# Kernel tuning notes

Hardware: AMD Instinct MI355X
Metric: run time of the kernel (lower is better)

Reference implementation:

```python
import jax, jax.numpy as jnp
import numpy as np

N_NODES = 50000
N_EDGES = 800000
BATCH = 128
D_IN = 768
D_H = 256
EPS_BN = 1e-5
EPS_COS = 1e-8


def setup_inputs() -> dict:
    key = jax.random.key(0)
    ks = jax.random.split(key, 16)
    s = 0.05
    return {
        "claim_embeddings": jax.random.normal(ks[0], (BATCH, D_IN), jnp.float32),
        "x": jax.random.normal(ks[1], (N_NODES, D_IN), jnp.float32),
        "edge_index": jax.random.randint(ks[2], (2, N_EDGES), 0, N_NODES, jnp.int32),
        "batch": jnp.sort(jax.random.randint(ks[3], (N_NODES,), 0, BATCH, jnp.int32)),
        "W1": jax.random.normal(ks[4], (D_IN, D_H), jnp.float32) * s,
        "a_src1": jax.random.normal(ks[5], (D_H,), jnp.float32) * s,
        "a_dst1": jax.random.normal(ks[6], (D_H,), jnp.float32) * s,
        "b1": jnp.zeros((D_H,), jnp.float32),
        "W2": jax.random.normal(ks[7], (D_H, D_H), jnp.float32) * s,
        "a_src2": jax.random.normal(ks[8], (D_H,), jnp.float32) * s,
        "a_dst2": jax.random.normal(ks[9], (D_H,), jnp.float32) * s,
        "b2": jnp.zeros((D_H,), jnp.float32),
        "bn_gamma": jnp.ones((D_H,), jnp.float32),
        "bn_beta": jnp.zeros((D_H,), jnp.float32),
        "Wc": jax.random.normal(ks[10], (D_H + D_IN, 1), jnp.float32) * s,
        "bc": jnp.zeros((1,), jnp.float32),
    }


def _gat_layer(h_in, src, dst, W, a_s, a_d, b, n_nodes):
    """PyG GATConv (heads=1, concat=True, self-loops already in src/dst)."""
    h = h_in @ W                                   # [N, D_H]
    alpha_s = h @ a_s                               # [N]
    alpha_d = h @ a_d                               # [N]
    e = jax.nn.leaky_relu(alpha_s[src] + alpha_d[dst], 0.2)  # [E+N]
    # numerically-stable softmax segmented by destination node
    e = e - jax.ops.segment_max(e, dst, num_segments=n_nodes)[dst]
    w = jnp.exp(e)
    w = w / jax.ops.segment_sum(w, dst, num_segments=n_nodes)[dst]
    out = jax.ops.segment_sum(h[src] * w[:, None], dst, num_segments=n_nodes)
    return out + b


def reference(claim_embeddings, x, edge_index, batch,
              W1, a_src1, a_dst1, b1, W2, a_src2, a_dst2, b2,
              bn_gamma, bn_beta, Wc, bc):
    n = x.shape[0]
    n_graphs = claim_embeddings.shape[0]
    # cosine-similarity relevance gating (torch eps semantics)
    ce = claim_embeddings[batch]                    # [N, D_IN]
    denom = jnp.maximum(jnp.linalg.norm(ce, axis=-1) * jnp.linalg.norm(x, axis=-1), EPS_COS)
    rel = jnp.sum(ce * x, axis=-1) / denom          # [N]
    h = x * rel[:, None]
    # add self-loops once (GATConv default add_self_loops=True)
    loops = jnp.arange(n, dtype=edge_index.dtype)
    src = jnp.concatenate([edge_index[0], loops])
    dst = jnp.concatenate([edge_index[1], loops])
    # layer 1 + batchnorm (batch stats) + relu
    h = _gat_layer(h, src, dst, W1, a_src1, a_dst1, b1, n)
    mean = jnp.mean(h, axis=0)
    var = jnp.mean(jnp.square(h - mean), axis=0)
    h = bn_gamma * (h - mean) * jax.lax.rsqrt(var + EPS_BN) + bn_beta
    h = jax.nn.relu(h)
    # layer 2 + relu
    h = _gat_layer(h, src, dst, W2, a_src2, a_dst2, b2, n)
    h = jax.nn.relu(h)
    # global mean pool per graph
    sums = jax.ops.segment_sum(h, batch, num_segments=n_graphs)
    counts = jax.ops.segment_sum(jnp.ones((n,), h.dtype), batch, num_segments=n_graphs)
    pooled = sums / jnp.maximum(counts, 1.0)[:, None]   # [B, D_H]
    combined = jnp.concatenate([pooled, claim_embeddings], axis=1)  # [B, D_H+D_IN]
    out = combined @ Wc + bc                        # [B, 1]
    return out.squeeze(-1)
```

## Files before the change

kernel.cpp:

```cpp
#include <hip/hip_runtime.h>
#include <hip/hip_bf16.h>

#define DIN 768
#define DH  256

typedef unsigned short ushort_t;
typedef unsigned char uchar_t;
typedef __attribute__((ext_vector_type(8))) short short8v;
typedef __attribute__((ext_vector_type(4))) float f32x4;
typedef __attribute__((ext_vector_type(2))) float f32x2;

__host__ __device__ inline int orig_col(int s) {
  int u = (s >> 2) & 31;
  return (s & ~127) | (((u >> 4) & 1) << 6) | ((s & 3) << 4) | (u & 15);
}

__device__ inline float wave_sum(float v) {
#pragma unroll
  for (int o = 32; o; o >>= 1) v += __shfl_xor(v, o);
  return v;
}
__device__ inline void wave_sum2(float& a, float& b) {
#pragma unroll
  for (int o = 32; o; o >>= 1) {
    a += __shfl_xor(a, o);
    b += __shfl_xor(b, o);
  }
}
__device__ inline float leaky(float v) { return v > 0.f ? v : 0.2f * v; }

__device__ inline ushort_t f2bf(float f) {
  union { float f; unsigned u; } v; v.f = f;
  unsigned r = v.u + 0x7FFFu + ((v.u >> 16) & 1u);
  return (ushort_t)(r >> 16);
}
__device__ inline float bf2f(ushort_t u) {
  union { unsigned u; float f; } t; t.u = ((unsigned)u) << 16; return t.f;
}

__device__ inline void unpack16f8(uint4 v, float* f) {
  f32x2 p;
  p = __builtin_amdgcn_cvt_pk_f32_fp8(v.x, false); f[0] = p[0]; f[1] = p[1];
  p = __builtin_amdgcn_cvt_pk_f32_fp8(v.x, true);  f[2] = p[0]; f[3] = p[1];
  p = __builtin_amdgcn_cvt_pk_f32_fp8(v.y, false); f[4] = p[0]; f[5] = p[1];
  p = __builtin_amdgcn_cvt_pk_f32_fp8(v.y, true);  f[6] = p[0]; f[7] = p[1];
  p = __builtin_amdgcn_cvt_pk_f32_fp8(v.z, false); f[8] = p[0]; f[9] = p[1];
  p = __builtin_amdgcn_cvt_pk_f32_fp8(v.z, true);  f[10] = p[0]; f[11] = p[1];
  p = __builtin_amdgcn_cvt_pk_f32_fp8(v.w, false); f[12] = p[0]; f[13] = p[1];
  p = __builtin_amdgcn_cvt_pk_f32_fp8(v.w, true);  f[14] = p[0]; f[15] = p[1];
}
__device__ inline uint4 pack8(const float* f) {
  uint4 o;
  o.x = (unsigned)f2bf(f[0]) | ((unsigned)f2bf(f[1]) << 16);
  o.y = (unsigned)f2bf(f[2]) | ((unsigned)f2bf(f[3]) << 16);
  o.z = (unsigned)f2bf(f[4]) | ((unsigned)f2bf(f[5]) << 16);
  o.w = (unsigned)f2bf(f[6]) | ((unsigned)f2bf(f[7]) << 16);
  return o;
}

__global__ __launch_bounds__(256) void relxb_hist_kernel(
    const float* __restrict__ ce, const float* __restrict__ x,
    const int* __restrict__ batch, const float* __restrict__ cenorm,
    ushort_t* __restrict__ xb, float* __restrict__ rel, int n,
    const int* __restrict__ edst, int E, int* __restrict__ cnt) {
  int node = blockIdx.x * 4 + (threadIdx.x >> 6);
  int lane = threadIdx.x & 63;
  if (node < n) {
    int g = batch[node];
    const float4* xr = (const float4*)(x + (size_t)node * DIN);
    const float4* cr = (const float4*)(ce + (size_t)g * DIN);
    float dxy = 0.f, dxx = 0.f;
#pragma unroll
    for (int i = 0; i < 3; i++) {
      float4 a = xr[lane + 64 * i];
      float4 b = cr[lane + 64 * i];
      ushort4 o = make_ushort4(f2bf(a.x), f2bf(a.y), f2bf(a.z), f2bf(a.w));
      *(ushort4*)&xb[(size_t)node * DIN + (lane + 64 * i) * 4] = o;
      dxy += a.x*b.x + a.y*b.y + a.z*b.z + a.w*b.w;
      dxx += a.x*a.x + a.y*a.y + a.z*a.z + a.w*a.w;
    }
    wave_sum2(dxy, dxx);
    if (lane == 0) {
      float denom = fmaxf(sqrtf(dxx) * cenorm[g], 1e-8f);
      rel[node] = dxy / denom;
    }
  }
  for (int e = blockIdx.x * blockDim.x + threadIdx.x; e < E;
       e += gridDim.x * blockDim.x)
    atomicAdd(&cnt[edst[e]], 1);
}

__global__ __launch_bounds__(256) void prep_kernel(
    const float* __restrict__ W1, const float* __restrict__ W2,
    const float* __restrict__ b1, const float* __restrict__ b2,
    const float* __restrict__ gamma, const float* __restrict__ beta,
    const float* __restrict__ Wc, const float* __restrict__ ce,
    ushort_t* __restrict__ Wt1, ushort_t* __restrict__ Wt2,
    float* __restrict__ pb1, float* __restrict__ pb2,
    float* __restrict__ pgamma, float* __restrict__ pbeta,
    float* __restrict__ pWc, float* __restrict__ cenorm, int B) {
  __shared__ float tile[64][65];
  int b = blockIdx.x;
  int t = threadIdx.x;
  int r4 = t >> 6;
  int c64 = t & 63;
  if (b < 48) {
    int k0 = (b % 12) * 64, c0 = (b / 12) * 64;
#pragma unroll
    for (int rr = 0; rr < 16; rr++) {
      int r = rr * 4 + r4;
      tile[r][c64] = W1[(size_t)(k0 + r) * 256 + c0 + c64];
    }
    __syncthreads();
#pragma unroll
    for (int rr = 0; rr < 16; rr++) {
      int cc = rr * 4 + r4;
      Wt1[(size_t)(c0 + cc) * DIN + k0 + c64] = f2bf(tile[c64][cc]);
    }
  } else if (b < 64) {
    int bb = b - 48;
    int k0 = (bb & 3) * 64, c0 = (bb >> 2) * 64;
#pragma unroll
    for (int rr = 0; rr < 16; rr++) {
      int r = rr * 4 + r4;
      tile[r][c64] = W2[(size_t)orig_col(k0 + r) * 256 + c0 + c64];
    }
    __syncthreads();
#pragma unroll
    for (int rr = 0; rr < 16; rr++) {
      int cc = rr * 4 + r4;
      Wt2[(size_t)(c0 + cc) * DH + k0 + c64] = f2bf(tile[c64][cc]);
    }
  } else if (b == 64) {
    int o = orig_col(t);
    pb1[t] = b1[o];
    pb2[t] = b2[o];
    pgamma[t] = gamma[o];
    pbeta[t] = beta[o];
    pWc[t] = Wc[o];
  } else {
    int lane = t & 63;
    for (int g = r4; g < B; g += 4) {
      const float4* cr = (const float4*)(ce + (size_t)g * DIN);
      float s = 0.f;
#pragma unroll
      for (int i = 0; i < 3; i++) {
        float4 v = cr[lane + 64 * i];
        s += v.x*v.x + v.y*v.y + v.z*v.z + v.w*v.w;
      }
      s = wave_sum(s);
      if (lane == 0) cenorm[g] = sqrtf(s);
    }
  }
}

__global__ __launch_bounds__(256) void scan1_kernel(const int* __restrict__ cnt,
                                                    int* __restrict__ row_off,
                                                    int* __restrict__ bsum, int n) {
  __shared__ int s[256];
  int t = threadIdx.x;
  int i = blockIdx.x * 256 + t;
  int v = (i < n) ? cnt[i] : 0;
  s[t] = v;
  __syncthreads();
  for (int off = 1; off < 256; off <<= 1) {
    int tmp = (t >= off) ? s[t - off] : 0;
    __syncthreads();
    s[t] += tmp;
    __syncthreads();
  }
  if (i < n) row_off[i] = s[t] - v;
  if (t == 255) bsum[blockIdx.x] = s[255];
}

__global__ __launch_bounds__(256) void scan2_kernel(const int* __restrict__ bsum,
                                                    int* __restrict__ boff, int nb,
                                                    int* __restrict__ row_off, int n) {
  __shared__ int s[256];
  int t = threadIdx.x;
  int v = (t < nb) ? bsum[t] : 0;
  s[t] = v;
  __syncthreads();
  for (int off = 1; off < 256; off <<= 1) {
    int tmp = (t >= off) ? s[t - off] : 0;
    __syncthreads();
    s[t] += tmp;
    __syncthreads();
  }
  if (t < nb) boff[t] = s[t] - v;
  if (t == nb - 1) row_off[n] = s[t];
}

__global__ __launch_bounds__(256) void scan3_kernel(int* __restrict__ row_off,
                                                    const int* __restrict__ boff, int n) {
  int i = blockIdx.x * 256 + threadIdx.x;
  if (i < n) row_off[i] += boff[blockIdx.x];
}

__global__ void fill_kernel(const int* __restrict__ src, const int* __restrict__ dst, int E,
                            const int* __restrict__ row_off, int* __restrict__ fill,
                            int* __restrict__ col_src) {
  for (int e = blockIdx.x * blockDim.x + threadIdx.x; e < E; e += gridDim.x * blockDim.x) {
    int d = dst[e];
    int slot = row_off[d] + atomicAdd(&fill[d], 1);
    col_src[slot] = src[e];
  }
}

template <int K>
__global__ __launch_bounds__(256) void gemm_mfma(
    const ushort_t* __restrict__ A, const ushort_t* __restrict__ Bt,
    uchar_t* __restrict__ C, const float* __restrict__ scale,
    const float* __restrict__ a_s, const float* __restrict__ a_d,
    float* __restrict__ alpha_s, float* __restrict__ alpha_d, int Mreal) {
  __shared__ ushort_t lds[16384];
  const int tid = threadIdx.x;
  const int lane = tid & 63;
  const int wave = tid >> 6;

  int p = blockIdx.y * 2 + blockIdx.x;
  int total = 2 * gridDim.y;
  int cch = p >> 4;
  int v;
  if ((cch << 4) + 16 <= total) {
    int r = p & 15;
    v = (cch << 4) | ((r & 7) << 1) | (r >> 3);
  } else {
    v = p;
  }
  const int col0 = (v & 1) * 128;
  const int row0 = (v >> 1) * 128;

  const int wr = wave >> 1, wc = wave & 1;
  const int c16 = lane & 15, g4 = lane >> 4;
  const int st_roff = lane >> 3;
  const int st_gsrc = (lane & 7) ^ st_roff;

  f32x4 acc[4][4];
#pragma unroll
  for (int m = 0; m < 4; m++)
#pragma unroll
    for (int nn = 0; nn < 4; nn++)
#pragma unroll
      for (int j = 0; j < 4; j++) acc[m][nn][j] = 0.f;

  for (int k0 = 0; k0 < K; k0 += 64) {
#pragma unroll
    for (int ci = 0; ci < 8; ci++) {
      int inst = wave * 8 + ci;
      int isB = inst >> 4;
      int idx = inst & 15;
      int lrow = idx * 8 + st_roff;
      const ushort_t* gsrc;
      if (isB == 0) {
        int rg = row0 + lrow;
        rg = rg < Mreal ? rg : Mreal - 1;
        gsrc = A + (size_t)rg * K + k0 + st_gsrc * 8;
      } else {
        gsrc = Bt + (size_t)(col0 + lrow) * K + k0 + st_gsrc * 8;
      }
      __builtin_amdgcn_global_load_lds(
          (const __attribute__((address_space(1))) void*)gsrc,
          (__attribute__((address_space(3))) void*)&lds[isB * 8192 + idx * 512],
          16, 0, 0);
    }
    __syncthreads();
#pragma unroll
    for (int ks = 0; ks < 2; ks++) {
      int g = ks * 4 + g4;
      short8v a[4], b[4];
#pragma unroll
      for (int m = 0; m < 4; m++) {
        int ra = wr * 64 + m * 16 + c16;
        a[m] = *(const short8v*)&lds[ra * 64 + (g ^ (ra & 7)) * 8];
      }
#pragma unroll
      for (int nn = 0; nn < 4; nn++) {
        int rb = wc * 64 + nn * 16 + c16;
        b[nn] = *(const short8v*)&lds[8192 + rb * 64 + (g ^ (rb & 7)) * 8];
      }
#pragma unroll
      for (int m = 0; m < 4; m++)
#pragma unroll
        for (int nn = 0; nn < 4; nn++)
          acc[m][nn] = __builtin_amdgcn_mfma_f32_16x16x32_bf16(a[m], b[nn],
                                                               acc[m][nn], 0, 0, 0);
    }
    __syncthreads();
  }

  float asv[4], adv[4];
#pragma unroll
  for (int nn = 0; nn < 4; nn++) {
    int col = col0 + wc * 64 + nn * 16 + c16;
    asv[nn] = a_s[col];
    adv[nn] = a_d[col];
  }

  uint* Cw = (uint*)C;
#pragma unroll
  for (int m = 0; m < 4; m++) {
    int row_base = row0 + wr * 64 + m * 16 + g4 * 4;
#pragma unroll
    for (int j = 0; j < 4; j++) {
      int row = row_base + j;
      int rc = row < Mreal ? row : Mreal - 1;
      float s = scale ? scale[rc] : 1.0f;
      float vs[4];
      float ps = 0.f, pd = 0.f;
#pragma unroll
      for (int nn = 0; nn < 4; nn++) {
        float v2 = acc[m][nn][j] * s;
        vs[nn] = v2;
        ps = fmaf(v2, asv[nn], ps);
        pd = fmaf(v2, adv[nn], pd);
      }
#pragma unroll
      for (int o = 1; o < 16; o <<= 1) {
        ps += __shfl_xor(ps, o);
        pd += __shfl_xor(pd, o);
      }
      if (c16 == 0 && row < Mreal) {
        atomicAdd(&alpha_s[row], ps);
        atomicAdd(&alpha_d[row], pd);
      }
      if (row < Mreal) {
        unsigned w8 = __builtin_amdgcn_cvt_pk_fp8_f32(vs[0], vs[1], 0u, false);
        w8 = __builtin_amdgcn_cvt_pk_fp8_f32(vs[2], vs[3], w8, true);
        Cw[(size_t)row * 64 + (col0 >> 2) + wc * 16 + c16] = w8;
      }
    }
  }
}

__global__ __launch_bounds__(256) void gat_agg(
    const uchar_t* __restrict__ h8, const float* __restrict__ as_,
    const float* __restrict__ ad_, const int* __restrict__ row_off,
    const int* __restrict__ col_src, const float* __restrict__ bias,
    ushort_t* __restrict__ outb, int n, int relu_out) {
  int node = blockIdx.x * 4 + (threadIdx.x >> 6);
  int lane = threadIdx.x & 63;
  if (node >= n) return;
  int lo = row_off[node], hi = row_off[node + 1];
  int deg = hi - lo;
  float adn = ad_[node];
  float w_self = __expf(leaky(as_[node] + adn));

  const int q = lane >> 4;
  const int l16 = lane & 15;
  const uchar_t* rowbase = h8 + (size_t)l16 * 16;

  float acc[16];
  float zacc = (lane == 0) ? w_self : 0.f;
  {
    uint4 v = *(const uint4*)(rowbase + (size_t)node * 256);
    float ws = (q == 0) ? w_self : 0.f;
    float f[16];
    unpack16f8(v, f);
#pragma unroll
    for (int i = 0; i < 16; i++) acc[i] = ws * f[i];
  }

  for (int base = 0; base < deg; base += 64) {
    int cnt = min(64, deg - base);
    int s = 0; float w = 0.f;
    if (lane < cnt) {
      s = col_src[lo + base + lane];
      w = __expf(leaky(as_[s] + adn));
    }
    zacc += w;
    int e = 0;
    for (; e + 8 <= cnt; e += 8) {
      int iA = e + q, iB = e + 4 + q;
      int sA = __shfl(s, iA);
      float wA = __shfl(w, iA);
      int sB = __shfl(s, iB);
      float wB = __shfl(w, iB);
      uint4 a0 = *(const uint4*)(rowbase + (size_t)sA * 256);
      uint4 b0 = *(const uint4*)(rowbase + (size_t)sB * 256);
      float f[16];
      unpack16f8(a0, f);
#pragma unroll
      for (int i = 0; i < 16; i++) acc[i] = fmaf(wA, f[i], acc[i]);
      unpack16f8(b0, f);
#pragma unroll
      for (int i = 0; i < 16; i++) acc[i] = fmaf(wB, f[i], acc[i]);
    }
    for (; e < cnt; e += 4) {
      int myE = e + q;
      int idx = myE < cnt ? myE : cnt - 1;
      int ss = __shfl(s, idx);
      float wv = __shfl(w, idx);
      float wgt = (myE < cnt) ? wv : 0.f;
      uint4 v = *(const uint4*)(rowbase + (size_t)ss * 256);
      float f[16];
      unpack16f8(v, f);
#pragma unroll
      for (int i = 0; i < 16; i++) acc[i] = fmaf(wgt, f[i], acc[i]);
    }
  }

  float z = wave_sum(zacc);
  float inv_z = 1.0f / z;

#pragma unroll
  for (int i = 0; i < 16; i++) {
    acc[i] += __shfl_xor(acc[i], 16);
    acc[i] += __shfl_xor(acc[i], 32);
  }

  if (q == 0) {
    float o[16];
#pragma unroll
    for (int i = 0; i < 16; i += 4) {
      float4 bb = *(const float4*)&bias[l16 * 16 + i];
      o[i]     = fmaf(acc[i],     inv_z, bb.x);
      o[i + 1] = fmaf(acc[i + 1], inv_z, bb.y);
      o[i + 2] = fmaf(acc[i + 2], inv_z, bb.z);
      o[i + 3] = fmaf(acc[i + 3], inv_z, bb.w);
    }
    if (relu_out) {
#pragma unroll
      for (int i = 0; i < 16; i++) o[i] = fmaxf(o[i], 0.f);
    }
    uint4* op = (uint4*)(outb + (size_t)node * 256 + l16 * 16);
    op[0] = pack8(o);
    op[1] = pack8(o + 8);
  }
}

__global__ __launch_bounds__(256) void bn_stats(const ushort_t* __restrict__ h, int n,
                                                float* __restrict__ bsum,
                                                float* __restrict__ bsq) {
  int c = threadIdx.x;
  int rows_per_block = (n + gridDim.x - 1) / gridDim.x;
  int r0 = blockIdx.x * rows_per_block;
  int r1 = min(r0 + rows_per_block, n);
  float sum = 0.f, sq = 0.f;
  for (int r = r0; r < r1; r++) {
    float v = bf2f(h[(size_t)r * 256 + c]);
    sum += v;
    sq = fmaf(v, v, sq);
  }
  atomicAdd(&bsum[c], sum);
  atomicAdd(&bsq[c], sq);
}

__global__ __launch_bounds__(256) void bn_apply(const ushort_t* __restrict__ h,
                                                const float* __restrict__ bsum,
                                                const float* __restrict__ bsq,
                                                const float* __restrict__ gamma,
                                                const float* __restrict__ beta,
                                                ushort_t* __restrict__ h2b, int n) {
  int total4 = n * 64;
  float inv_n = 1.0f / (float)n;
  for (int f = blockIdx.x * blockDim.x + threadIdx.x; f < total4;
       f += gridDim.x * blockDim.x) {
    int c4 = f & 63;
    uint2 hv = ((const uint2*)h)[f];
    float v0, v1, v2, v3;
    {
      union { unsigned u; float fl; } t;
      t.u = hv.x << 16;         v0 = t.fl;
      t.u = hv.x & 0xFFFF0000u; v1 = t.fl;
      t.u = hv.y << 16;         v2 = t.fl;
      t.u = hv.y & 0xFFFF0000u; v3 = t.fl;
    }
    float4 sm = ((const float4*)bsum)[c4];
    float4 sl = ((const float4*)bsq)[c4];
    float4 g = ((const float4*)gamma)[c4];
    float4 bb = ((const float4*)beta)[c4];
    float m, var;
    m = sm.x * inv_n; var = sl.x * inv_n - m * m;
    v0 = fmaxf(g.x * (v0 - m) * rsqrtf(var + 1e-5f) + bb.x, 0.f);
    m = sm.y * inv_n; var = sl.y * inv_n - m * m;
    v1 = fmaxf(g.y * (v1 - m) * rsqrtf(var + 1e-5f) + bb.y, 0.f);
    m = sm.z * inv_n; var = sl.z * inv_n - m * m;
    v2 = fmaxf(g.z * (v2 - m) * rsqrtf(var + 1e-5f) + bb.z, 0.f);
    m = sm.w * inv_n; var = sl.w * inv_n - m * m;
    v3 = fmaxf(g.w * (v3 - m) * rsqrtf(var + 1e-5f) + bb.w, 0.f);
    uint2 o;
    o.x = (unsigned)f2bf(v0) | ((unsigned)f2bf(v1) << 16);
    o.y = (unsigned)f2bf(v2) | ((unsigned)f2bf(v3) << 16);
    ((uint2*)h2b)[f] = o;
  }
}

__device__ inline int lower_bound_dev(const int* a, int n, int v) {
  int lo = 0, hi = n;
  while (lo < hi) {
    int mid = (lo + hi) >> 1;
    if (a[mid] < v) lo = mid + 1; else hi = mid;
  }
  return lo;
}

#define POOL_CHUNKS 16
__global__ __launch_bounds__(256) void pool_partial(const ushort_t* __restrict__ h,
                                                    const int* __restrict__ batch, int n,
                                                    float* __restrict__ psum) {
  int g = blockIdx.x / POOL_CHUNKS;
  int c = blockIdx.x % POOL_CHUNKS;
  int lo = lower_bound_dev(batch, n, g);
  int hi = lower_bound_dev(batch, n, g + 1);
  int len = hi - lo;
  int r0 = lo + (int)(((long long)len * c) / POOL_CHUNKS);
  int r1 = lo + (int)(((long long)len * (c + 1)) / POOL_CHUNKS);
  if (r1 <= r0) return;
  float sum = 0.f;
  for (int r = r0; r < r1; r++) sum += bf2f(h[(size_t)r * 256 + threadIdx.x]);
  atomicAdd(&psum[(size_t)g * 256 + threadIdx.x], sum);
}

__global__ __launch_bounds__(256) void final_kernel(const float* __restrict__ psum,
                                                    const int* __restrict__ batch, int n,
                                                    const float* __restrict__ ce,
                                                    const float* __restrict__ pWc,
                                                    const float* __restrict__ Wc,
                                                    const float* __restrict__ bc,
                                                    float* __restrict__ out, int B) {
  int g = blockIdx.x;
  int t = threadIdx.x;
  int lo = lower_bound_dev(batch, n, g);
  int hi = lower_bound_dev(batch, n, g + 1);
  float inv_cnt = 1.0f / fmaxf((float)(hi - lo), 1.0f);
  float p = 0.f;
  p = fmaf(psum[(size_t)g * 256 + t] * inv_cnt, pWc[t], p);
  p = fmaf(ce[(size_t)g * 768 + t],        Wc[256 + t], p);
  p = fmaf(ce[(size_t)g * 768 + 256 + t],  Wc[512 + t], p);
  p = fmaf(ce[(size_t)g * 768 + 512 + t],  Wc[768 + t], p);
  __shared__ float red[256];
  red[t] = p;
  __syncthreads();
  for (int s = 128; s; s >>= 1) {
    if (t < s) red[t] += red[t + s];
    __syncthreads();
  }
  if (t == 0) out[g] = red[0] + bc[0];
}

extern "C" void kernel_launch(void* const* d_in, const int* in_sizes, int n_in,
                              void* d_out, int out_size, void* d_ws, size_t ws_size,
                              hipStream_t stream) {
  const float* ce    = (const float*)d_in[0];
  const float* x     = (const float*)d_in[1];
  const int*   edge  = (const int*)d_in[2];
  const int*   batch = (const int*)d_in[3];
  const float* W1    = (const float*)d_in[4];
  const float* a_s1  = (const float*)d_in[5];
  const float* a_d1  = (const float*)d_in[6];
  const float* b1    = (const float*)d_in[7];
  const float* W2    = (const float*)d_in[8];
  const float* a_s2  = (const float*)d_in[9];
  const float* a_d2  = (const float*)d_in[10];
  const float* b2    = (const float*)d_in[11];
  const float* gamma = (const float*)d_in[12];
  const float* beta  = (const float*)d_in[13];
  const float* Wc    = (const float*)d_in[14];
  const float* bc    = (const float*)d_in[15];

  const int B = in_sizes[0] / DIN;
  const int n = in_sizes[1] / DIN;
  const int E = in_sizes[2] / 2;
  const int* esrc = edge;
  const int* edst = edge + E;

  char* w = (char*)d_ws;
  size_t off = 0;
  auto carve = [&](size_t bytes) -> void* {
    void* p = w + off;
    off = (off + bytes + 255) & ~(size_t)255;
    return p;
  };
  size_t hbytes  = (size_t)n * DH * 2;
  size_t h8bytes = (size_t)n * DH;
  char*  R1      = (char*)carve((size_t)n * DIN * 2);
  ushort_t* xb    = (ushort_t*)R1;
  ushort_t* h1b   = (ushort_t*)R1;
  ushort_t* h2b   = (ushort_t*)(R1 + hbytes);
  ushort_t* buf_ob = (ushort_t*)(R1 + 2 * hbytes);
  uchar_t* buf_h8 = (uchar_t*)carve(h8bytes);
  int*   row_off = (int*)carve((size_t)(n + 1) * 4);
  int*   col_src = (int*)carve((size_t)E * 4);
  ushort_t* Wt1  = (ushort_t*)carve((size_t)DIN * DH * 2);
  ushort_t* Wt2  = (ushort_t*)carve((size_t)DH * DH * 2);
  float* pb1     = (float*)carve(DH * 4);
  float* pb2     = (float*)carve(DH * 4);
  float* pgamma  = (float*)carve(DH * 4);
  float* pbeta   = (float*)carve(DH * 4);
  float* pWc     = (float*)carve(DH * 4);
  float* cenorm  = (float*)carve((size_t)B * 4);
  float* rel     = (float*)carve((size_t)n * 4);
  int*   sc_bsum = (int*)carve(256 * 4);
  int*   sc_boff = (int*)carve(256 * 4);
  char* zero0 = (char*)carve((size_t)n * 4);
  int*   cnt     = (int*)zero0;
  int*   fill    = (int*)carve((size_t)n * 4);
  float* as1buf  = (float*)carve((size_t)n * 4);
  float* ad1buf  = (float*)carve((size_t)n * 4);
  float* as2buf  = (float*)carve((size_t)n * 4);
  float* ad2buf  = (float*)carve((size_t)n * 4);
  float* bn_sum  = (float*)carve(DH * 4);
  float* bn_sq   = (float*)carve(DH * 4);
  float* psum    = (float*)carve((size_t)B * DH * 4);
  size_t zero_bytes = (size_t)((char*)(psum + (size_t)B * DH) - zero0);

  hipMemsetAsync(zero0, 0, zero_bytes, stream);

  const int gN4 = (n + 3) / 4;
  const int Mb = (n + 127) / 128;
  const int nb = (n + 255) / 256;

  prep_kernel<<<66, 256, 0, stream>>>(W1, W2, b1, b2, gamma, beta, Wc, ce,
                                      Wt1, Wt2, pb1, pb2, pgamma, pbeta, pWc,
                                      cenorm, B);
  relxb_hist_kernel<<<gN4, 256, 0, stream>>>(ce, x, batch, cenorm, xb, rel, n,
                                             edst, E, cnt);
  scan1_kernel<<<nb, 256, 0, stream>>>(cnt, row_off, sc_bsum, n);
  scan2_kernel<<<1, 256, 0, stream>>>(sc_bsum, sc_boff, nb, row_off, n);
  scan3_kernel<<<nb, 256, 0, stream>>>(row_off, sc_boff, n);
  fill_kernel<<<1024, 256, 0, stream>>>(esrc, edst, E, row_off, fill, col_src);

  gemm_mfma<DIN><<<dim3(2, Mb), 256, 0, stream>>>(xb, Wt1, buf_h8, rel, a_s1,
                                                  a_d1, as1buf, ad1buf, n);
  gat_agg<<<gN4, 256, 0, stream>>>(buf_h8, as1buf, ad1buf, row_off, col_src, pb1,
                                   h1b, n, 0);
  bn_stats<<<512, 256, 0, stream>>>(h1b, n, bn_sum, bn_sq);
  bn_apply<<<2048, 256, 0, stream>>>(h1b, bn_sum, bn_sq, pgamma, pbeta, h2b, n);

  gemm_mfma<DH><<<dim3(2, Mb), 256, 0, stream>>>(h2b, Wt2, buf_h8, nullptr, a_s2,
                                                 a_d2, as2buf, ad2buf, n);
  gat_agg<<<gN4, 256, 0, stream>>>(buf_h8, as2buf, ad2buf, row_off, col_src, pb2,
                                   buf_ob, n, 1);

  pool_partial<<<B * POOL_CHUNKS, 256, 0, stream>>>(buf_ob, batch, n, psum);
  final_kernel<<<B, 256, 0, stream>>>(psum, batch, n, ce, pWc, Wc, bc,
                                      (float*)d_out, B);
}
```

Measured before the change: 378.4 us.

## Feed fp32 x directly into layer-1 GEMM, converting to bf16 in-kernel

Stops writing a bf16 copy of x in the relevance/histogram kernel. Adds a new layer-1 GEMM that loads fp32 x tiles straight into LDS and converts them to bf16 in registers before the MFMA. This removes a 77 MB bf16 write and its read back from HBM. In exchange the GEMM reads twice as many A bytes (fp32), needs more LDS and does extra conversion work per tile, and x is still read twice overall.

```diff
diff --git a/kernel.cpp b/kernel.cpp
--- a/kernel.cpp
+++ b/kernel.cpp
@@ -36,6 +36,15 @@
 }
 __device__ inline float bf2f(ushort_t u) {
   union { unsigned u; float f; } t; t.u = ((unsigned)u) << 16; return t.f;
+}
+
+__device__ inline short8v cvt8bf(const float* f) {
+  union { short8v s; unsigned u[4]; } r;
+#pragma unroll
+  for (int i = 0; i < 4; i++)
+    asm("v_cvt_pk_bf16_f32 %0, %1, %2"
+        : "=v"(r.u[i]) : "v"(f[2 * i]), "v"(f[2 * i + 1]));
+  return r.s;
 }
 
 __device__ inline void unpack16f8(uint4 v, float* f) {
@@ -58,10 +67,10 @@
   return o;
 }
 
-__global__ __launch_bounds__(256) void relxb_hist_kernel(
+__global__ __launch_bounds__(256) void rel_hist_kernel(
     const float* __restrict__ ce, const float* __restrict__ x,
     const int* __restrict__ batch, const float* __restrict__ cenorm,
-    ushort_t* __restrict__ xb, float* __restrict__ rel, int n,
+    float* __restrict__ rel, int n,
     const int* __restrict__ edst, int E, int* __restrict__ cnt) {
   int node = blockIdx.x * 4 + (threadIdx.x >> 6);
   int lane = threadIdx.x & 63;
@@ -74,8 +83,6 @@
     for (int i = 0; i < 3; i++) {
       float4 a = xr[lane + 64 * i];
       float4 b = cr[lane + 64 * i];
-      ushort4 o = make_ushort4(f2bf(a.x), f2bf(a.y), f2bf(a.z), f2bf(a.w));
-      *(ushort4*)&xb[(size_t)node * DIN + (lane + 64 * i) * 4] = o;
       dxy += a.x*b.x + a.y*b.y + a.z*b.z + a.w*b.w;
       dxx += a.x*a.x + a.y*a.y + a.z*a.z + a.w*a.w;
     }
@@ -204,6 +211,138 @@
     int d = dst[e];
     int slot = row_off[d] + atomicAdd(&fill[d], 1);
     col_src[slot] = src[e];
+  }
+}
+
+__global__ __launch_bounds__(256) void gemm_mfma_f32A(
+    const float* __restrict__ A, const ushort_t* __restrict__ Bt,
+    uchar_t* __restrict__ C, const float* __restrict__ scale,
+    const float* __restrict__ a_s, const float* __restrict__ a_d,
+    float* __restrict__ alpha_s, float* __restrict__ alpha_d, int Mreal) {
+  constexpr int K = DIN;
+  __shared__ float ldsA[8192];
+  __shared__ ushort_t ldsB[8192];
+  const int tid = threadIdx.x;
+  const int lane = tid & 63;
+  const int wave = tid >> 6;
+
+  int p = blockIdx.y * 2 + blockIdx.x;
+  int total = 2 * gridDim.y;
+  int cch = p >> 4;
+  int v;
+  if ((cch << 4) + 16 <= total) {
+    int r = p & 15;
+    v = (cch << 4) | ((r & 7) << 1) | (r >> 3);
+  } else {
+    v = p;
+  }
+  const int col0 = (v & 1) * 128;
+  const int row0 = (v >> 1) * 128;
+
+  const int wr = wave >> 1, wc = wave & 1;
+  const int c16 = lane & 15, g4 = lane >> 4;
+
+  f32x4 acc[4][4];
+#pragma unroll
+  for (int m = 0; m < 4; m++)
+#pragma unroll
+    for (int nn = 0; nn < 4; nn++)
+#pragma unroll
+      for (int j = 0; j < 4; j++) acc[m][nn][j] = 0.f;
+
+  for (int k0 = 0; k0 < K; k0 += 64) {
+#pragma unroll
+    for (int ci = 0; ci < 12; ci++) {
+      int inst = wave * 12 + ci;
+      if (inst < 32) {
+        int lrow = inst * 4 + (lane >> 4);
+        int rg = row0 + lrow;
+        rg = rg < Mreal ? rg : Mreal - 1;
+        int ksrc = (lane & 15) ^ (lrow & 15);
+        const float* gsrc = A + (size_t)rg * K + k0 + ksrc * 4;
+        __builtin_amdgcn_global_load_lds(
+            (const __attribute__((address_space(1))) void*)gsrc,
+            (__attribute__((address_space(3))) void*)&ldsA[inst * 256], 16, 0, 0);
+      } else {
+        int j = inst - 32;
+        int lrow = j * 8 + (lane >> 3);
+        int ksrc = (lane & 7) ^ (lrow & 7);
+        const ushort_t* gsrc = Bt + (size_t)(col0 + lrow) * K + k0 + ksrc * 8;
+        __builtin_amdgcn_global_load_lds(
+            (const __attribute__((address_space(1))) void*)gsrc,
+            (__attribute__((address_space(3))) void*)&ldsB[j * 512], 16, 0, 0);
+      }
+    }
+    __syncthreads();
+#pragma unroll
+    for (int ks = 0; ks < 2; ks++) {
+      int g = ks * 4 + g4;
+      short8v a[4], b[4];
+#pragma unroll
+      for (int m = 0; m < 4; m++) {
+        int ra = wr * 64 + m * 16 + c16;
+        int sw = ra & 15;
+        const float4 lo4 = *(const float4*)&ldsA[(ra * 16 + ((2 * g) ^ sw)) * 4];
+        const float4 hi4 = *(const float4*)&ldsA[(ra * 16 + ((2 * g + 1) ^ sw)) * 4];
+        float f[8] = {lo4.x, lo4.y, lo4.z, lo4.w, hi4.x, hi4.y, hi4.z, hi4.w};
+        a[m] = cvt8bf(f);
+      }
+#pragma unroll
+      for (int nn = 0; nn < 4; nn++) {
+        int rb = wc * 64 + nn * 16 + c16;
+        b[nn] = *(const short8v*)&ldsB[rb * 64 + (g ^ (rb & 7)) * 8];
+      }
+#pragma unroll
+      for (int m = 0; m < 4; m++)
+#pragma unroll
+        for (int nn = 0; nn < 4; nn++)
+          acc[m][nn] = __builtin_amdgcn_mfma_f32_16x16x32_bf16(a[m], b[nn],
+                                                               acc[m][nn], 0, 0, 0);
+    }
+    __syncthreads();
+  }
+
+  float asv[4], adv[4];
+#pragma unroll
+  for (int nn = 0; nn < 4; nn++) {
+    int col = col0 + wc * 64 + nn * 16 + c16;
+    asv[nn] = a_s[col];
+    adv[nn] = a_d[col];
+  }
+
+  uint* Cw = (uint*)C;
+#pragma unroll
+  for (int m = 0; m < 4; m++) {
+    int row_base = row0 + wr * 64 + m * 16 + g4 * 4;
+#pragma unroll
+    for (int j = 0; j < 4; j++) {
+      int row = row_base + j;
+      int rc = row < Mreal ? row : Mreal - 1;
+      float s = scale ? scale[rc] : 1.0f;
+      float vs[4];
+      float ps = 0.f, pd = 0.f;
+#pragma unroll
+      for (int nn = 0; nn < 4; nn++) {
+        float v2 = acc[m][nn][j] * s;
+        vs[nn] = v2;
+        ps = fmaf(v2, asv[nn], ps);
+        pd = fmaf(v2, adv[nn], pd);
+      }
+#pragma unroll
+      for (int o = 1; o < 16; o <<= 1) {
+        ps += __shfl_xor(ps, o);
+        pd += __shfl_xor(pd, o);
+      }
+      if (c16 == 0 && row < Mreal) {
+        atomicAdd(&alpha_s[row], ps);
+        atomicAdd(&alpha_d[row], pd);
+      }
+      if (row < Mreal) {
+        unsigned w8 = __builtin_amdgcn_cvt_pk_fp8_f32(vs[0], vs[1], 0u, false);
+        w8 = __builtin_amdgcn_cvt_pk_fp8_f32(vs[2], vs[3], w8, true);
+        Cw[(size_t)row * 64 + (col0 >> 2) + wc * 16 + c16] = w8;
+      }
+    }
   }
 }
 
@@ -574,11 +713,9 @@
   };
   size_t hbytes  = (size_t)n * DH * 2;
   size_t h8bytes = (size_t)n * DH;
-  char*  R1      = (char*)carve((size_t)n * DIN * 2);
-  ushort_t* xb    = (ushort_t*)R1;
-  ushort_t* h1b   = (ushort_t*)R1;
-  ushort_t* h2b   = (ushort_t*)(R1 + hbytes);
-  ushort_t* buf_ob = (ushort_t*)(R1 + 2 * hbytes);
+  ushort_t* h1b   = (ushort_t*)carve(hbytes);
+  ushort_t* h2b   = (ushort_t*)carve(hbytes);
+  ushort_t* buf_ob = (ushort_t*)carve(hbytes);
   uchar_t* buf_h8 = (uchar_t*)carve(h8bytes);
   int*   row_off = (int*)carve((size_t)(n + 1) * 4);
   int*   col_src = (int*)carve((size_t)E * 4);
@@ -614,14 +751,14 @@
   prep_kernel<<<66, 256, 0, stream>>>(W1, W2, b1, b2, gamma, beta, Wc, ce,
                                       Wt1, Wt2, pb1, pb2, pgamma, pbeta, pWc,
                                       cenorm, B);
-  relxb_hist_kernel<<<gN4, 256, 0, stream>>>(ce, x, batch, cenorm, xb, rel, n,
-                                             edst, E, cnt);
+  rel_hist_kernel<<<gN4, 256, 0, stream>>>(ce, x, batch, cenorm, rel, n,
+                                           edst, E, cnt);
   scan1_kernel<<<nb, 256, 0, stream>>>(cnt, row_off, sc_bsum, n);
   scan2_kernel<<<1, 256, 0, stream>>>(sc_bsum, sc_boff, nb, row_off, n);
   scan3_kernel<<<nb, 256, 0, stream>>>(row_off, sc_boff, n);
   fill_kernel<<<1024, 256, 0, stream>>>(esrc, edst, E, row_off, fill, col_src);
 
-  gemm_mfma<DIN><<<dim3(2, Mb), 256, 0, stream>>>(xb, Wt1, buf_h8, rel, a_s1,
+  gemm_mfma_f32A<<<dim3(2, Mb), 256, 0, stream>>>(x, Wt1, buf_h8, rel, a_s1,
                                                   a_d1, as1buf, ad1buf, n);
   gat_agg<<<gN4, 256, 0, stream>>>(buf_h8, as1buf, ad1buf, row_off, col_src, pb1,
                                    h1b, n, 0);
```

Measured after the change: 378.5 us. About the same (+0.0%).
